# Kernel tuning notes

Measured on AMD Instinct MI355X. Metric: run time of the kernel, lower is better.

The kernel has to match this reference:

```python
import jax, jax.numpy as jnp
import numpy as np

N = 100000      # nodes
E = 1600000     # edges (avg degree 16)
D_IN = 128
D_OUT = 128
ALPHA = 0.2     # leaky-relu negative slope
EPS = 1e-8


def setup_inputs() -> dict:
    key = jax.random.key(0)
    kx, kr, kc, kW, ka = jax.random.split(key, 5)
    x = jax.random.normal(kx, (N, D_IN), dtype=jnp.float32)
    row = jax.random.randint(kr, (E,), 0, N)
    col = jax.random.randint(kc, (E,), 0, N)
    stdv_w = 1.0 / np.sqrt(D_OUT)
    W = jax.random.uniform(kW, (D_IN, D_OUT), jnp.float32, -stdv_w, stdv_w)
    stdv_a = 1.0 / np.sqrt(2 * D_OUT)
    a = jax.random.uniform(ka, (2 * D_OUT, 1), jnp.float32, -stdv_a, stdv_a)
    return {"x": x, "row": row, "col": col, "W": W, "a": a}


def reference(x, row, col, W, a):
    # h = x W : [N, D_OUT]
    h = x @ W
    n = x.shape[0]
    # a is applied to cat([h_row, h_col]); split so we never materialize [E, 2*D_OUT]:
    # e_ij = leaky_relu(h_i . a[:D] + h_j . a[D:])
    s_src = h @ a[:D_OUT, 0]   # [N]
    s_dst = h @ a[D_OUT:, 0]   # [N]
    e = s_src[row] + s_dst[col]               # [E]
    e = jnp.where(e > 0, e, ALPHA * e)        # leaky relu
    # segment (per-row) softmax, numerically stable
    row_max = jax.ops.segment_max(e, row, num_segments=n)
    e_exp = jnp.exp(e - row_max[row])
    row_sum = jax.ops.segment_sum(e_exp, row, num_segments=n)
    row_sum = jnp.maximum(row_sum, EPS)       # clamp(min=1e-8)
    att = e_exp / row_sum[row]                # [E]
    # sparse.mm(attention, h): scatter-add of att * h[col] into rows
    h_prime = jax.ops.segment_sum(att[:, None] * h[col], row, num_segments=n)
    # concat=True -> elu
    return jax.nn.elu(h_prime)
```

## Files before the change

### kernel.cpp

```cpp
#include <hip/hip_runtime.h>
#include <cstddef>

#define ALPHA 0.2f
#define EPS 1e-8f
#define LOG_RPB 6
#define RPB 64
#define COL_BITS 17
#define COL_MASK 0x1FFFFu
#define CAP 2048
#define MAXBIN 2048
#define SCHUNK 8192

typedef __attribute__((ext_vector_type(8))) short short8v;
typedef __attribute__((ext_vector_type(4))) float f32x4;

static __device__ __forceinline__ unsigned short f2bf(float f) {
  unsigned int u = __float_as_uint(f);
  unsigned int r = u + 0x7fffu + ((u >> 16) & 1u);
  return (unsigned short)(r >> 16);
}
static __device__ __forceinline__ float bf2f(unsigned short s) {
  return __uint_as_float(((unsigned int)s) << 16);
}
static __device__ __forceinline__ float rlanef(float v, int l) {
  return __uint_as_float(__builtin_amdgcn_readlane(__float_as_uint(v), l));
}

__global__ __launch_bounds__(256) void wt_prep_kernel(
    const float* __restrict__ W, unsigned short* __restrict__ wt) {
  int idx = blockIdx.x * 256 + threadIdx.x;
  int nn = idx >> 7, k = idx & 127;
  wt[idx] = f2bf(W[k * 128 + nn]);
}

__global__ __launch_bounds__(256) void gemm_scores_kernel(
    const float* __restrict__ x, const unsigned short* __restrict__ wt,
    const float* __restrict__ a, unsigned short* __restrict__ h_bf,
    float* __restrict__ s_src, float* __restrict__ s_dst, int n) {
  __shared__ unsigned short c_lds[64][128];
  const int t = threadIdx.x;
  const int w = t >> 6, lane = t & 63;
  const int n16 = lane & 15, g = lane >> 4;
  const int row0 = blockIdx.x * 64 + w * 16;
  int arow = row0 + n16;
  if (arow >= n) arow = n - 1;

  f32x4 acc[8];
#pragma unroll
  for (int cf = 0; cf < 8; cf++) acc[cf] = (f32x4){0.f, 0.f, 0.f, 0.f};

#pragma unroll
  for (int s = 0; s < 4; s++) {
    const int k0 = s * 32 + g * 8;
    const float* xr = x + (size_t)arow * 128 + k0;
    float4 av0 = ((const float4*)xr)[0];
    float4 av1 = ((const float4*)xr)[1];
    short8v afrag;
    afrag[0] = (short)f2bf(av0.x); afrag[1] = (short)f2bf(av0.y);
    afrag[2] = (short)f2bf(av0.z); afrag[3] = (short)f2bf(av0.w);
    afrag[4] = (short)f2bf(av1.x); afrag[5] = (short)f2bf(av1.y);
    afrag[6] = (short)f2bf(av1.z); afrag[7] = (short)f2bf(av1.w);
#pragma unroll
    for (int cf = 0; cf < 8; cf++) {
      short8v bfrag = *(const short8v*)(wt + (size_t)(cf * 16 + n16) * 128 + k0);
      acc[cf] = __builtin_amdgcn_mfma_f32_16x16x32_bf16(afrag, bfrag, acc[cf], 0, 0, 0);
    }
  }

  float p0[4] = {0.f, 0.f, 0.f, 0.f}, p1[4] = {0.f, 0.f, 0.f, 0.f};
#pragma unroll
  for (int cf = 0; cf < 8; cf++) {
    const int col = cf * 16 + n16;
    const float a0 = a[col], a1 = a[128 + col];
#pragma unroll
    for (int j = 0; j < 4; j++) {
      float v = acc[cf][j];
      c_lds[w * 16 + g * 4 + j][col] = f2bf(v);
      p0[j] += v * a0;
      p1[j] += v * a1;
    }
  }
#pragma unroll
  for (int j = 0; j < 4; j++) {
#pragma unroll
    for (int off = 1; off <= 8; off <<= 1) {
      p0[j] += __shfl_xor(p0[j], off, 64);
      p1[j] += __shfl_xor(p1[j], off, 64);
    }
  }
  if (n16 == 0) {
#pragma unroll
    for (int j = 0; j < 4; j++) {
      int r = row0 + g * 4 + j;
      if (r < n) { s_src[r] = p0[j]; s_dst[r] = p1[j]; }
    }
  }
  __syncthreads();
  {
    int row = t >> 2, q = t & 3;
    int nid = blockIdx.x * 64 + row;
    if (nid < n) {
      const uint4* src = (const uint4*)&c_lds[row][q * 32];
      uint4 v0 = src[0], v1 = src[1], v2 = src[2], v3 = src[3];
      uint4* dst = (uint4*)&h_bf[(size_t)nid * 128 + q * 32];
      dst[0] = v0; dst[1] = v1; dst[2] = v2; dst[3] = v3;
    }
  }
}

__global__ __launch_bounds__(256) void binscatter_kernel(
    const int* __restrict__ row, const int* __restrict__ col,
    int* __restrict__ bin_count, unsigned int* __restrict__ packed,
    int E, int nbin) {
  __shared__ int hist[MAXBIN];
  const int t = threadIdx.x;
  for (int b = t; b < nbin; b += 256) hist[b] = 0;
  __syncthreads();

  const int e0 = blockIdx.x * SCHUNK;
  const int eend = (e0 + SCHUNK < E) ? e0 + SCHUNK : E;

  for (int i = e0 + t * 4; i < eend; i += 1024) {
    if (i + 3 < eend) {
      int4 v = *(const int4*)&row[i];
      atomicAdd(&hist[v.x >> LOG_RPB], 1);
      atomicAdd(&hist[v.y >> LOG_RPB], 1);
      atomicAdd(&hist[v.z >> LOG_RPB], 1);
      atomicAdd(&hist[v.w >> LOG_RPB], 1);
    } else {
      for (int j = 0; j < 4 && i + j < eend; j++)
        atomicAdd(&hist[row[i + j] >> LOG_RPB], 1);
    }
  }
  __syncthreads();

  for (int b = t; b < nbin; b += 256) {
    int cnt = hist[b];
    hist[b] = cnt ? atomicAdd(&bin_count[b], cnt) : 0;
  }
  __syncthreads();

  for (int i = e0 + t * 4; i < eend; i += 1024) {
    if (i + 3 < eend) {
      int4 rv = *(const int4*)&row[i];
      int4 cv = *(const int4*)&col[i];
      int b0 = rv.x >> LOG_RPB, b1 = rv.y >> LOG_RPB;
      int b2 = rv.z >> LOG_RPB, b3 = rv.w >> LOG_RPB;
      int q0 = atomicAdd(&hist[b0], 1);
      int q1 = atomicAdd(&hist[b1], 1);
      int q2 = atomicAdd(&hist[b2], 1);
      int q3 = atomicAdd(&hist[b3], 1);
      if (q0 < CAP) packed[(size_t)b0 * CAP + q0] =
          ((unsigned int)(rv.x & (RPB - 1)) << COL_BITS) | ((unsigned int)cv.x & COL_MASK);
      if (q1 < CAP) packed[(size_t)b1 * CAP + q1] =
          ((unsigned int)(rv.y & (RPB - 1)) << COL_BITS) | ((unsigned int)cv.y & COL_MASK);
      if (q2 < CAP) packed[(size_t)b2 * CAP + q2] =
          ((unsigned int)(rv.z & (RPB - 1)) << COL_BITS) | ((unsigned int)cv.z & COL_MASK);
      if (q3 < CAP) packed[(size_t)b3 * CAP + q3] =
          ((unsigned int)(rv.w & (RPB - 1)) << COL_BITS) | ((unsigned int)cv.w & COL_MASK);
    } else {
      for (int j = 0; j < 4 && i + j < eend; j++) {
        int r = row[i + j], c = col[i + j];
        int b = r >> LOG_RPB;
        int q = atomicAdd(&hist[b], 1);
        if (q < CAP) packed[(size_t)b * CAP + q] =
            ((unsigned int)(r & (RPB - 1)) << COL_BITS) | ((unsigned int)c & COL_MASK);
      }
    }
  }
}

__global__ __launch_bounds__(512) void attend_bin_kernel(
    const ushort2* __restrict__ h2, const unsigned int* __restrict__ packed,
    const int* __restrict__ bin_count, const float* __restrict__ s_src,
    const float* __restrict__ s_dst, float* __restrict__ out, int n) {
  __shared__ unsigned int scol[CAP];
  __shared__ int rowbase[RPB + 1];
  __shared__ int cursor[RPB];
  __shared__ int hist[RPB];

  const int bin = blockIdx.x;
  const size_t start = (size_t)bin * CAP;
  int cnt = bin_count[bin];
  if (cnt > CAP) cnt = CAP;
  const int t = threadIdx.x;
  const int wave = t >> 6;
  const int lane = t & 63;

  if (t < RPB) hist[t] = 0;
  __syncthreads();
  for (int i = t; i < cnt; i += 512)
    atomicAdd(&hist[packed[start + i] >> COL_BITS], 1);
  __syncthreads();
  if (t < RPB) cursor[t] = hist[t];
  __syncthreads();
  for (int off = 1; off < RPB; off <<= 1) {
    int y = (t < RPB && t >= off) ? cursor[t - off] : 0;
    __syncthreads();
    if (t < RPB) cursor[t] += y;
    __syncthreads();
  }
  if (t < RPB) rowbase[t + 1] = cursor[t];
  if (t == 0) rowbase[0] = 0;
  __syncthreads();
  if (t < RPB) cursor[t] = rowbase[t];
  __syncthreads();
  for (int i = t; i < cnt; i += 512) {
    unsigned int u = packed[start + i];
    int pos = atomicAdd(&cursor[u >> COL_BITS], 1);
    scol[pos] = u & COL_MASK;
  }
  __syncthreads();

  for (int rr = 0; rr < 8; ++rr) {
    const int lr = wave * 8 + rr;
    const int r = (bin << LOG_RPB) + lr;
    if (r >= n) continue;
    const float sr = s_src[r];
    float acc0 = 0.f, acc1 = 0.f, ssum = 0.f;
    const int rs = rowbase[lr];
    const int deg = rowbase[lr + 1] - rs;

    for (int b2 = 0; b2 < deg; b2 += 64) {
      const int rem = deg - b2;
      const bool act = lane < rem;
      int c = act ? (int)scol[rs + b2 + lane] : 0;
      float p = 0.f;
      if (act) {
        float ev = sr + s_dst[c];
        ev = ev > 0.f ? ev : ALPHA * ev;
        p = __expf(ev);
      }
      float cs = p;
#pragma unroll
      for (int off = 32; off >= 1; off >>= 1) cs += __shfl_xor(cs, off, 64);
      ssum += cs;

      const int knt = rem < 64 ? rem : 64;
      int k = 0;
      for (; k + 8 <= knt; k += 8) {
        float pp[8];
        int cc[8];
        ushort2 vv[8];
#pragma unroll
        for (int i = 0; i < 8; i++) {
          pp[i] = rlanef(p, k + i);
          cc[i] = __builtin_amdgcn_readlane(c, k + i);
        }
#pragma unroll
        for (int i = 0; i < 8; i++) vv[i] = h2[(size_t)cc[i] * 64 + lane];
#pragma unroll
        for (int i = 0; i < 8; i++) {
          acc0 += pp[i] * bf2f(vv[i].x);
          acc1 += pp[i] * bf2f(vv[i].y);
        }
      }
      for (; k + 4 <= knt; k += 4) {
        float pp[4];
        int cc[4];
        ushort2 vv[4];
#pragma unroll
        for (int i = 0; i < 4; i++) {
          pp[i] = rlanef(p, k + i);
          cc[i] = __builtin_amdgcn_readlane(c, k + i);
        }
#pragma unroll
        for (int i = 0; i < 4; i++) vv[i] = h2[(size_t)cc[i] * 64 + lane];
#pragma unroll
        for (int i = 0; i < 4; i++) {
          acc0 += pp[i] * bf2f(vv[i].x);
          acc1 += pp[i] * bf2f(vv[i].y);
        }
      }
      for (; k < knt; ++k) {
        float pk = rlanef(p, k);
        int ck = __builtin_amdgcn_readlane(c, k);
        ushort2 v = h2[(size_t)ck * 64 + lane];
        acc0 += pk * bf2f(v.x);
        acc1 += pk * bf2f(v.y);
      }
    }

    float inv = 1.0f / fmaxf(ssum, EPS);
    acc0 *= inv; acc1 *= inv;
    float o0 = acc0 > 0.f ? acc0 : expm1f(acc0);
    float o1 = acc1 > 0.f ? acc1 : expm1f(acc1);
    *(float2*)&out[(size_t)r * 128 + lane * 2] = make_float2(o0, o1);
  }
}

static inline size_t align256(size_t v) { return (v + 255) & ~(size_t)255; }

extern "C" void kernel_launch(void* const* d_in, const int* in_sizes, int n_in,
                              void* d_out, int out_size, void* d_ws, size_t ws_size,
                              hipStream_t stream) {
  const float* x   = (const float*)d_in[0];
  const int*   row = (const int*)d_in[1];
  const int*   col = (const int*)d_in[2];
  const float* W   = (const float*)d_in[3];
  const float* a   = (const float*)d_in[4];
  float* out = (float*)d_out;

  const int N = in_sizes[0] / 128;
  const int E = in_sizes[1];
  const int NBIN = (N + RPB - 1) >> LOG_RPB;

  char* ws = (char*)d_ws;
  unsigned short* h_bf = (unsigned short*)ws; ws += align256((size_t)N * 128 * 2);
  unsigned short* wt   = (unsigned short*)ws; ws += align256((size_t)128 * 128 * 2);
  float* s_src     = (float*)ws;       ws += align256((size_t)N * 4);
  float* s_dst     = (float*)ws;       ws += align256((size_t)N * 4);
  int*   bin_count = (int*)ws;         ws += align256((size_t)NBIN * 4);
  unsigned int* packed = (unsigned int*)ws; ws += align256((size_t)NBIN * CAP * 4);

  hipMemsetAsync(bin_count, 0, (size_t)NBIN * 4, stream);

  dim3 blk(256);
  wt_prep_kernel<<<dim3(64), blk, 0, stream>>>(W, wt);
  gemm_scores_kernel<<<dim3((N + 63) / 64), blk, 0, stream>>>(
      x, wt, a, h_bf, s_src, s_dst, N);
  binscatter_kernel<<<dim3((E + SCHUNK - 1) / SCHUNK), blk, 0, stream>>>(
      row, col, bin_count, packed, E, NBIN);
  attend_bin_kernel<<<dim3(NBIN), dim3(512), 0, stream>>>(
      (const ushort2*)h_bf, packed, bin_count, s_src, s_dst, out, N);
}
```

Baseline: 147.5 us.

## Fuse GEMM with edge bin-scatter and precompute edge weights during LDS sort

Merges the GEMM/score kernel and the edge binning kernel into one launch, with every eighth GEMM block also running grid-strided edge-chunk scatter. This removes a kernel boundary and lets the scatter overlap the GEMM. In the attend kernel, attention exponentials are computed once per edge while sorting into LDS and stored beside a pre-scaled byte offset. The gather loop then reads from LDS instead of using readlane broadcasts and per-chunk wave reductions. The row-offset scan now uses a wave shuffle scan instead of a barrier-heavy LDS scan. The tradeoffs are doubled LDS for the edge array, fewer blocks doing the scatter, and a per-lane serial ssum.

```diff
diff --git a/kernel.cpp b/kernel.cpp
--- a/kernel.cpp
+++ b/kernel.cpp
@@ -22,9 +22,6 @@
 static __device__ __forceinline__ float bf2f(unsigned short s) {
   return __uint_as_float(((unsigned int)s) << 16);
 }
-static __device__ __forceinline__ float rlanef(float v, int l) {
-  return __uint_as_float(__builtin_amdgcn_readlane(__float_as_uint(v), l));
-}
 
 __global__ __launch_bounds__(256) void wt_prep_kernel(
     const float* __restrict__ W, unsigned short* __restrict__ wt) {
@@ -33,151 +30,158 @@
   wt[idx] = f2bf(W[k * 128 + nn]);
 }
 
-__global__ __launch_bounds__(256) void gemm_scores_kernel(
+__global__ __launch_bounds__(256) void gemm_scatter_kernel(
     const float* __restrict__ x, const unsigned short* __restrict__ wt,
-    const float* __restrict__ a, unsigned short* __restrict__ h_bf,
-    float* __restrict__ s_src, float* __restrict__ s_dst, int n) {
+    const float* __restrict__ a, const int* __restrict__ row,
+    const int* __restrict__ col, unsigned short* __restrict__ h_bf,
+    float* __restrict__ s_src, float* __restrict__ s_dst,
+    int* __restrict__ bin_count, unsigned int* __restrict__ packed,
+    int n, int E, int nbin) {
   __shared__ unsigned short c_lds[64][128];
-  const int t = threadIdx.x;
-  const int w = t >> 6, lane = t & 63;
-  const int n16 = lane & 15, g = lane >> 4;
-  const int row0 = blockIdx.x * 64 + w * 16;
-  int arow = row0 + n16;
-  if (arow >= n) arow = n - 1;
-
-  f32x4 acc[8];
-#pragma unroll
-  for (int cf = 0; cf < 8; cf++) acc[cf] = (f32x4){0.f, 0.f, 0.f, 0.f};
-
-#pragma unroll
-  for (int s = 0; s < 4; s++) {
-    const int k0 = s * 32 + g * 8;
-    const float* xr = x + (size_t)arow * 128 + k0;
-    float4 av0 = ((const float4*)xr)[0];
-    float4 av1 = ((const float4*)xr)[1];
-    short8v afrag;
-    afrag[0] = (short)f2bf(av0.x); afrag[1] = (short)f2bf(av0.y);
-    afrag[2] = (short)f2bf(av0.z); afrag[3] = (short)f2bf(av0.w);
-    afrag[4] = (short)f2bf(av1.x); afrag[5] = (short)f2bf(av1.y);
-    afrag[6] = (short)f2bf(av1.z); afrag[7] = (short)f2bf(av1.w);
-#pragma unroll
-    for (int cf = 0; cf < 8; cf++) {
-      short8v bfrag = *(const short8v*)(wt + (size_t)(cf * 16 + n16) * 128 + k0);
-      acc[cf] = __builtin_amdgcn_mfma_f32_16x16x32_bf16(afrag, bfrag, acc[cf], 0, 0, 0);
-    }
-  }
-
-  float p0[4] = {0.f, 0.f, 0.f, 0.f}, p1[4] = {0.f, 0.f, 0.f, 0.f};
-#pragma unroll
-  for (int cf = 0; cf < 8; cf++) {
-    const int col = cf * 16 + n16;
-    const float a0 = a[col], a1 = a[128 + col];
-#pragma unroll
-    for (int j = 0; j < 4; j++) {
-      float v = acc[cf][j];
-      c_lds[w * 16 + g * 4 + j][col] = f2bf(v);
-      p0[j] += v * a0;
-      p1[j] += v * a1;
-    }
-  }
-#pragma unroll
-  for (int j = 0; j < 4; j++) {
-#pragma unroll
-    for (int off = 1; off <= 8; off <<= 1) {
-      p0[j] += __shfl_xor(p0[j], off, 64);
-      p1[j] += __shfl_xor(p1[j], off, 64);
-    }
-  }
-  if (n16 == 0) {
-#pragma unroll
-    for (int j = 0; j < 4; j++) {
-      int r = row0 + g * 4 + j;
-      if (r < n) { s_src[r] = p0[j]; s_dst[r] = p1[j]; }
-    }
-  }
-  __syncthreads();
-  {
-    int row = t >> 2, q = t & 3;
-    int nid = blockIdx.x * 64 + row;
-    if (nid < n) {
-      const uint4* src = (const uint4*)&c_lds[row][q * 32];
-      uint4 v0 = src[0], v1 = src[1], v2 = src[2], v3 = src[3];
-      uint4* dst = (uint4*)&h_bf[(size_t)nid * 128 + q * 32];
-      dst[0] = v0; dst[1] = v1; dst[2] = v2; dst[3] = v3;
-    }
-  }
-}
-
-__global__ __launch_bounds__(256) void binscatter_kernel(
-    const int* __restrict__ row, const int* __restrict__ col,
-    int* __restrict__ bin_count, unsigned int* __restrict__ packed,
-    int E, int nbin) {
   __shared__ int hist[MAXBIN];
   const int t = threadIdx.x;
-  for (int b = t; b < nbin; b += 256) hist[b] = 0;
-  __syncthreads();
-
-  const int e0 = blockIdx.x * SCHUNK;
-  const int eend = (e0 + SCHUNK < E) ? e0 + SCHUNK : E;
-
-  for (int i = e0 + t * 4; i < eend; i += 1024) {
-    if (i + 3 < eend) {
-      int4 v = *(const int4*)&row[i];
-      atomicAdd(&hist[v.x >> LOG_RPB], 1);
-      atomicAdd(&hist[v.y >> LOG_RPB], 1);
-      atomicAdd(&hist[v.z >> LOG_RPB], 1);
-      atomicAdd(&hist[v.w >> LOG_RPB], 1);
-    } else {
-      for (int j = 0; j < 4 && i + j < eend; j++)
-        atomicAdd(&hist[row[i + j] >> LOG_RPB], 1);
-    }
-  }
-  __syncthreads();
-
-  for (int b = t; b < nbin; b += 256) {
-    int cnt = hist[b];
-    hist[b] = cnt ? atomicAdd(&bin_count[b], cnt) : 0;
-  }
-  __syncthreads();
-
-  for (int i = e0 + t * 4; i < eend; i += 1024) {
-    if (i + 3 < eend) {
-      int4 rv = *(const int4*)&row[i];
-      int4 cv = *(const int4*)&col[i];
-      int b0 = rv.x >> LOG_RPB, b1 = rv.y >> LOG_RPB;
-      int b2 = rv.z >> LOG_RPB, b3 = rv.w >> LOG_RPB;
-      int q0 = atomicAdd(&hist[b0], 1);
-      int q1 = atomicAdd(&hist[b1], 1);
-      int q2 = atomicAdd(&hist[b2], 1);
-      int q3 = atomicAdd(&hist[b3], 1);
-      if (q0 < CAP) packed[(size_t)b0 * CAP + q0] =
-          ((unsigned int)(rv.x & (RPB - 1)) << COL_BITS) | ((unsigned int)cv.x & COL_MASK);
-      if (q1 < CAP) packed[(size_t)b1 * CAP + q1] =
-          ((unsigned int)(rv.y & (RPB - 1)) << COL_BITS) | ((unsigned int)cv.y & COL_MASK);
-      if (q2 < CAP) packed[(size_t)b2 * CAP + q2] =
-          ((unsigned int)(rv.z & (RPB - 1)) << COL_BITS) | ((unsigned int)cv.z & COL_MASK);
-      if (q3 < CAP) packed[(size_t)b3 * CAP + q3] =
-          ((unsigned int)(rv.w & (RPB - 1)) << COL_BITS) | ((unsigned int)cv.w & COL_MASK);
-    } else {
-      for (int j = 0; j < 4 && i + j < eend; j++) {
-        int r = row[i + j], c = col[i + j];
-        int b = r >> LOG_RPB;
-        int q = atomicAdd(&hist[b], 1);
-        if (q < CAP) packed[(size_t)b * CAP + q] =
-            ((unsigned int)(r & (RPB - 1)) << COL_BITS) | ((unsigned int)c & COL_MASK);
+
+  {
+    const int w = t >> 6, lane = t & 63;
+    const int n16 = lane & 15, g = lane >> 4;
+    const int row0 = blockIdx.x * 64 + w * 16;
+    int arow = row0 + n16;
+    if (arow >= n) arow = n - 1;
+
+    f32x4 acc[8];
+#pragma unroll
+    for (int cf = 0; cf < 8; cf++) acc[cf] = (f32x4){0.f, 0.f, 0.f, 0.f};
+
+#pragma unroll
+    for (int s = 0; s < 4; s++) {
+      const int k0 = s * 32 + g * 8;
+      const float* xr = x + (size_t)arow * 128 + k0;
+      float4 av0 = ((const float4*)xr)[0];
+      float4 av1 = ((const float4*)xr)[1];
+      short8v afrag;
+      afrag[0] = (short)f2bf(av0.x); afrag[1] = (short)f2bf(av0.y);
+      afrag[2] = (short)f2bf(av0.z); afrag[3] = (short)f2bf(av0.w);
+      afrag[4] = (short)f2bf(av1.x); afrag[5] = (short)f2bf(av1.y);
+      afrag[6] = (short)f2bf(av1.z); afrag[7] = (short)f2bf(av1.w);
+#pragma unroll
+      for (int cf = 0; cf < 8; cf++) {
+        short8v bfrag = *(const short8v*)(wt + (size_t)(cf * 16 + n16) * 128 + k0);
+        acc[cf] = __builtin_amdgcn_mfma_f32_16x16x32_bf16(afrag, bfrag, acc[cf], 0, 0, 0);
+      }
+    }
+
+    float p0[4] = {0.f, 0.f, 0.f, 0.f}, p1[4] = {0.f, 0.f, 0.f, 0.f};
+#pragma unroll
+    for (int cf = 0; cf < 8; cf++) {
+      const int colx = cf * 16 + n16;
+      const float a0 = a[colx], a1 = a[128 + colx];
+#pragma unroll
+      for (int j = 0; j < 4; j++) {
+        float v = acc[cf][j];
+        c_lds[w * 16 + g * 4 + j][colx] = f2bf(v);
+        p0[j] += v * a0;
+        p1[j] += v * a1;
+      }
+    }
+#pragma unroll
+    for (int j = 0; j < 4; j++) {
+#pragma unroll
+      for (int off = 1; off <= 8; off <<= 1) {
+        p0[j] += __shfl_xor(p0[j], off, 64);
+        p1[j] += __shfl_xor(p1[j], off, 64);
+      }
+    }
+    if (n16 == 0) {
+#pragma unroll
+      for (int j = 0; j < 4; j++) {
+        int r = row0 + g * 4 + j;
+        if (r < n) { s_src[r] = p0[j]; s_dst[r] = p1[j]; }
+      }
+    }
+    __syncthreads();
+    {
+      int rw = t >> 2, q = t & 3;
+      int nid = blockIdx.x * 64 + rw;
+      if (nid < n) {
+        const uint4* src = (const uint4*)&c_lds[rw][q * 32];
+        uint4 v0 = src[0], v1 = src[1], v2 = src[2], v3 = src[3];
+        uint4* dst = (uint4*)&h_bf[(size_t)nid * 128 + q * 32];
+        dst[0] = v0; dst[1] = v1; dst[2] = v2; dst[3] = v3;
+      }
+    }
+  }
+
+  if ((blockIdx.x & 7) != 0) return;
+  const int CHUNKS = (E + SCHUNK - 1) / SCHUNK;
+  const int STRIDE8 = (gridDim.x + 7) >> 3;
+  for (int ch = blockIdx.x >> 3; ch < CHUNKS; ch += STRIDE8) {
+    __syncthreads();
+    for (int b = t; b < nbin; b += 256) hist[b] = 0;
+    __syncthreads();
+
+    const int e0 = ch * SCHUNK;
+    const int eend = (e0 + SCHUNK < E) ? e0 + SCHUNK : E;
+
+    for (int i = e0 + t * 4; i < eend; i += 1024) {
+      if (i + 3 < eend) {
+        int4 v = *(const int4*)&row[i];
+        atomicAdd(&hist[v.x >> LOG_RPB], 1);
+        atomicAdd(&hist[v.y >> LOG_RPB], 1);
+        atomicAdd(&hist[v.z >> LOG_RPB], 1);
+        atomicAdd(&hist[v.w >> LOG_RPB], 1);
+      } else {
+        for (int j = 0; j < 4 && i + j < eend; j++)
+          atomicAdd(&hist[row[i + j] >> LOG_RPB], 1);
+      }
+    }
+    __syncthreads();
+
+    for (int b = t; b < nbin; b += 256) {
+      int cnt = hist[b];
+      hist[b] = cnt ? atomicAdd(&bin_count[b], cnt) : 0;
+    }
+    __syncthreads();
+
+    for (int i = e0 + t * 4; i < eend; i += 1024) {
+      if (i + 3 < eend) {
+        int4 rv = *(const int4*)&row[i];
+        int4 cv = *(const int4*)&col[i];
+        int b0 = rv.x >> LOG_RPB, b1 = rv.y >> LOG_RPB;
+        int b2 = rv.z >> LOG_RPB, b3 = rv.w >> LOG_RPB;
+        int q0 = atomicAdd(&hist[b0], 1);
+        int q1 = atomicAdd(&hist[b1], 1);
+        int q2 = atomicAdd(&hist[b2], 1);
+        int q3 = atomicAdd(&hist[b3], 1);
+        if (q0 < CAP) packed[(size_t)b0 * CAP + q0] =
+            ((unsigned int)(rv.x & (RPB - 1)) << COL_BITS) | ((unsigned int)cv.x & COL_MASK);
+        if (q1 < CAP) packed[(size_t)b1 * CAP + q1] =
+            ((unsigned int)(rv.y & (RPB - 1)) << COL_BITS) | ((unsigned int)cv.y & COL_MASK);
+        if (q2 < CAP) packed[(size_t)b2 * CAP + q2] =
+            ((unsigned int)(rv.z & (RPB - 1)) << COL_BITS) | ((unsigned int)cv.z & COL_MASK);
+        if (q3 < CAP) packed[(size_t)b3 * CAP + q3] =
+            ((unsigned int)(rv.w & (RPB - 1)) << COL_BITS) | ((unsigned int)cv.w & COL_MASK);
+      } else {
+        for (int j = 0; j < 4 && i + j < eend; j++) {
+          int r = row[i + j], c = col[i + j];
+          int b = r >> LOG_RPB;
+          int q = atomicAdd(&hist[b], 1);
+          if (q < CAP) packed[(size_t)b * CAP + q] =
+              ((unsigned int)(r & (RPB - 1)) << COL_BITS) | ((unsigned int)c & COL_MASK);
+        }
       }
     }
   }
 }
 
 __global__ __launch_bounds__(512) void attend_bin_kernel(
-    const ushort2* __restrict__ h2, const unsigned int* __restrict__ packed,
+    const unsigned short* __restrict__ h_bf, const unsigned int* __restrict__ packed,
     const int* __restrict__ bin_count, const float* __restrict__ s_src,
     const float* __restrict__ s_dst, float* __restrict__ out, int n) {
-  __shared__ unsigned int scol[CAP];
+  __shared__ uint2 ep[CAP];
+  __shared__ float s_row[RPB];
+  __shared__ int hist[RPB];
+  __shared__ int cursor[RPB];
   __shared__ int rowbase[RPB + 1];
-  __shared__ int cursor[RPB];
-  __shared__ int hist[RPB];
 
   const int bin = blockIdx.x;
   const size_t start = (size_t)bin * CAP;
@@ -187,98 +191,93 @@
   const int wave = t >> 6;
   const int lane = t & 63;
 
-  if (t < RPB) hist[t] = 0;
+  if (t < RPB) {
+    hist[t] = 0;
+    int r = (bin << LOG_RPB) + t;
+    s_row[t] = (r < n) ? s_src[r] : 0.f;
+  }
   __syncthreads();
+
   for (int i = t; i < cnt; i += 512)
     atomicAdd(&hist[packed[start + i] >> COL_BITS], 1);
   __syncthreads();
-  if (t < RPB) cursor[t] = hist[t];
+
+  if (wave == 0) {
+    int orig = hist[lane];
+    int v = orig;
+#pragma unroll
+    for (int off = 1; off < 64; off <<= 1) {
+      int y = __shfl_up(v, off, 64);
+      if (lane >= off) v += y;
+    }
+    rowbase[lane + 1] = v;
+    int excl = v - orig;
+    cursor[lane] = excl;
+    if (lane == 0) rowbase[0] = 0;
+  }
   __syncthreads();
-  for (int off = 1; off < RPB; off <<= 1) {
-    int y = (t < RPB && t >= off) ? cursor[t - off] : 0;
-    __syncthreads();
-    if (t < RPB) cursor[t] += y;
-    __syncthreads();
-  }
-  if (t < RPB) rowbase[t + 1] = cursor[t];
-  if (t == 0) rowbase[0] = 0;
-  __syncthreads();
-  if (t < RPB) cursor[t] = rowbase[t];
-  __syncthreads();
+
   for (int i = t; i < cnt; i += 512) {
     unsigned int u = packed[start + i];
-    int pos = atomicAdd(&cursor[u >> COL_BITS], 1);
-    scol[pos] = u & COL_MASK;
+    int lr = (int)(u >> COL_BITS);
+    int c = (int)(u & COL_MASK);
+    float ev = s_row[lr] + s_dst[c];
+    ev = ev > 0.f ? ev : ALPHA * ev;
+    float p = __expf(ev);
+    int pos = atomicAdd(&cursor[lr], 1);
+    ep[pos] = make_uint2((unsigned int)c << 8, __float_as_uint(p));
   }
   __syncthreads();
 
+  const char* hlane = (const char*)h_bf + (size_t)(lane << 2);
   for (int rr = 0; rr < 8; ++rr) {
     const int lr = wave * 8 + rr;
     const int r = (bin << LOG_RPB) + lr;
     if (r >= n) continue;
-    const float sr = s_src[r];
-    float acc0 = 0.f, acc1 = 0.f, ssum = 0.f;
     const int rs = rowbase[lr];
     const int deg = rowbase[lr + 1] - rs;
-
-    for (int b2 = 0; b2 < deg; b2 += 64) {
-      const int rem = deg - b2;
-      const bool act = lane < rem;
-      int c = act ? (int)scol[rs + b2 + lane] : 0;
-      float p = 0.f;
-      if (act) {
-        float ev = sr + s_dst[c];
-        ev = ev > 0.f ? ev : ALPHA * ev;
-        p = __expf(ev);
-      }
-      float cs = p;
-#pragma unroll
-      for (int off = 32; off >= 1; off >>= 1) cs += __shfl_xor(cs, off, 64);
-      ssum += cs;
-
-      const int knt = rem < 64 ? rem : 64;
-      int k = 0;
-      for (; k + 8 <= knt; k += 8) {
-        float pp[8];
-        int cc[8];
-        ushort2 vv[8];
-#pragma unroll
-        for (int i = 0; i < 8; i++) {
-          pp[i] = rlanef(p, k + i);
-          cc[i] = __builtin_amdgcn_readlane(c, k + i);
-        }
-#pragma unroll
-        for (int i = 0; i < 8; i++) vv[i] = h2[(size_t)cc[i] * 64 + lane];
-#pragma unroll
-        for (int i = 0; i < 8; i++) {
-          acc0 += pp[i] * bf2f(vv[i].x);
-          acc1 += pp[i] * bf2f(vv[i].y);
-        }
-      }
-      for (; k + 4 <= knt; k += 4) {
-        float pp[4];
-        int cc[4];
-        ushort2 vv[4];
-#pragma unroll
-        for (int i = 0; i < 4; i++) {
-          pp[i] = rlanef(p, k + i);
-          cc[i] = __builtin_amdgcn_readlane(c, k + i);
-        }
-#pragma unroll
-        for (int i = 0; i < 4; i++) vv[i] = h2[(size_t)cc[i] * 64 + lane];
-#pragma unroll
-        for (int i = 0; i < 4; i++) {
-          acc0 += pp[i] * bf2f(vv[i].x);
-          acc1 += pp[i] * bf2f(vv[i].y);
-        }
-      }
-      for (; k < knt; ++k) {
-        float pk = rlanef(p, k);
-        int ck = __builtin_amdgcn_readlane(c, k);
-        ushort2 v = h2[(size_t)ck * 64 + lane];
-        acc0 += pk * bf2f(v.x);
-        acc1 += pk * bf2f(v.y);
-      }
+    float acc0 = 0.f, acc1 = 0.f, ssum = 0.f;
+
+    int k = 0;
+    for (; k + 8 <= deg; k += 8) {
+      uint2 e[8];
+      ushort2 v[8];
+#pragma unroll
+      for (int i = 0; i < 8; i++) e[i] = ep[rs + k + i];
+#pragma unroll
+      for (int i = 0; i < 8; i++)
+        v[i] = *(const ushort2*)(hlane + e[i].x);
+#pragma unroll
+      for (int i = 0; i < 8; i++) {
+        float p = __uint_as_float(e[i].y);
+        ssum += p;
+        acc0 += p * bf2f(v[i].x);
+        acc1 += p * bf2f(v[i].y);
+      }
+    }
+    for (; k + 4 <= deg; k += 4) {
+      uint2 e[4];
+      ushort2 v[4];
+#pragma unroll
+      for (int i = 0; i < 4; i++) e[i] = ep[rs + k + i];
+#pragma unroll
+      for (int i = 0; i < 4; i++)
+        v[i] = *(const ushort2*)(hlane + e[i].x);
+#pragma unroll
+      for (int i = 0; i < 4; i++) {
+        float p = __uint_as_float(e[i].y);
+        ssum += p;
+        acc0 += p * bf2f(v[i].x);
+        acc1 += p * bf2f(v[i].y);
+      }
+    }
+    for (; k < deg; ++k) {
+      uint2 e = ep[rs + k];
+      ushort2 v = *(const ushort2*)(hlane + e.x);
+      float p = __uint_as_float(e.y);
+      ssum += p;
+      acc0 += p * bf2f(v.x);
+      acc1 += p * bf2f(v.y);
     }
 
     float inv = 1.0f / fmaxf(ssum, EPS);
@@ -304,6 +303,7 @@
   const int N = in_sizes[0] / 128;
   const int E = in_sizes[1];
   const int NBIN = (N + RPB - 1) >> LOG_RPB;
+  const int NBG = (N + 63) / 64;
 
   char* ws = (char*)d_ws;
   unsigned short* h_bf = (unsigned short*)ws; ws += align256((size_t)N * 128 * 2);
@@ -317,10 +317,8 @@
 
   dim3 blk(256);
   wt_prep_kernel<<<dim3(64), blk, 0, stream>>>(W, wt);
-  gemm_scores_kernel<<<dim3((N + 63) / 64), blk, 0, stream>>>(
-      x, wt, a, h_bf, s_src, s_dst, N);
-  binscatter_kernel<<<dim3((E + SCHUNK - 1) / SCHUNK), blk, 0, stream>>>(
-      row, col, bin_count, packed, E, NBIN);
+  gemm_scatter_kernel<<<dim3(NBG), blk, 0, stream>>>(
+      x, wt, a, row, col, h_bf, s_src, s_dst, bin_count, packed, N, E, NBIN);
   attend_bin_kernel<<<dim3(NBIN), dim3(512), 0, stream>>>(
-      (const ushort2*)h_bf, packed, bin_count, s_src, s_dst, out, N);
-}
+      h_bf, packed, bin_count, s_src, s_dst, out, N);
+}
```

New measurement: 203.2 us. +37.8%, slower.
